# Optimization experiments

Measured on AMD Instinct MI355X. Metric: run time of the kernel, lower is better.

The kernel has to match this reference:

```python
import jax, jax.numpy as jnp
import numpy as np

B, T, D, H = 4, 2048, 512, 8
DH = D // H  # 64
EPS = 1e-5


def setup_inputs() -> dict:
    key = jax.random.key(0)
    ks = jax.random.split(key, 12)
    s = lambda k, shp, fan: jax.random.normal(k, shp, jnp.float32) * (fan ** -0.5)
    return {
        "x": jax.random.normal(ks[0], (B, T, D), jnp.float32),
        "ln1_g": jnp.ones((D,), jnp.float32),
        "ln1_b": jnp.zeros((D,), jnp.float32),
        "Wq": s(ks[1], (H, D, DH), D),  # per-head bias-free projections
        "Wk": s(ks[2], (H, D, DH), D),
        "Wv": s(ks[3], (H, D, DH), D),
        "Wproj": s(ks[4], (D, D), D),
        "bproj": jnp.zeros((D,), jnp.float32),
        "W1": s(ks[5], (D, 4 * D), D),
        "b1": jnp.zeros((4 * D,), jnp.float32),
        "W2": s(ks[6], (4 * D, D), 4 * D),
        "b2": jnp.zeros((D,), jnp.float32),
    }


def _layernorm(x, g, b):
    m = jnp.mean(x, axis=-1, keepdims=True)
    v = jnp.var(x, axis=-1, keepdims=True)
    return (x - m) * jax.lax.rsqrt(v + EPS) * g + b


def reference(x, ln1_g, ln1_b, Wq, Wk, Wv, Wproj, bproj, W1, b1, W2, b2):
    b, t, c = x.shape
    scale = c ** -0.5  # source scales by input channel dim, not head_size
    causal = jnp.tril(jnp.ones((t, t), bool))  # [T,T]

    # --- attention sublayer (pre-norm with ln1) ---
    h = _layernorm(x, ln1_g, ln1_b)
    q = jnp.einsum('btd,hde->bhte', h, Wq)
    k = jnp.einsum('btd,hde->bhte', h, Wk)
    v = jnp.einsum('btd,hde->bhte', h, Wv)
    scores = jnp.einsum('bhte,bhse->bhts', q, k) * scale  # [B,H,T,T]
    scores = jnp.where(causal, scores, -jnp.inf)
    att = jax.nn.softmax(scores, axis=-1)  # dropout = identity at inference
    o = jnp.einsum('bhts,bhse->bthe', att, v).reshape(b, t, c)  # concat heads
    sa = o @ Wproj + bproj
    x = x + sa

    # --- FFN sublayer (source reuses ln1, faithful) ---
    h2 = _layernorm(x, ln1_g, ln1_b)
    ff = jax.nn.relu(h2 @ W1 + b1) @ W2 + b2
    return x + ff
```

## Files before the change

### kernel.cpp

```cpp
#include <hip/hip_runtime.h>
#include <math.h>

#define B_ 4
#define T_ 2048
#define D_ 512
#define H_ 8
#define DH_ 64
#define BT_ 8192
#define FF_ 2048
#define EPS_ 1e-5f
#define SCALE_ 0.04419417382415922f
#define SC2_ 0.06375861151f
#define NEGINF_ -1e30f

typedef short b16x8 __attribute__((ext_vector_type(8)));
typedef short b16x4 __attribute__((ext_vector_type(4)));
typedef float f32x4 __attribute__((ext_vector_type(4)));

#define MFMA16(a, b, c) __builtin_amdgcn_mfma_f32_16x16x32_bf16(a, b, c, 0, 0, 0)
#define MFMA16K16(a, b, c) __builtin_amdgcn_mfma_f32_16x16x16bf16_1k(a, b, c, 0, 0, 0)

#define GLL16(gp, lp) \
    __builtin_amdgcn_global_load_lds((const __attribute__((address_space(1))) void*)(gp), \
                                     (__attribute__((address_space(3))) void*)(lp), 16, 0, 0)

#if __has_builtin(__builtin_amdgcn_exp2f)
#define EXP2F(x) __builtin_amdgcn_exp2f(x)
#else
#define EXP2F(x) exp2f(x)
#endif

static __device__ inline short f2bf(float f) {
    unsigned int u = __builtin_bit_cast(unsigned int, f);
    unsigned int r = (u + 0x7fffu + ((u >> 16) & 1u)) >> 16;
    return (short)r;
}
static __device__ inline short f2bf_trunc(float f) {
    return (short)(__builtin_bit_cast(unsigned int, f) >> 16);
}
static __device__ inline float bf2f(short s) {
    return __builtin_bit_cast(float, ((unsigned int)(unsigned short)s) << 16);
}

__global__ __launch_bounds__(256) void prologue_kernel(
        const float* __restrict__ Wq, const float* __restrict__ Wk,
        const float* __restrict__ Wv, const float* __restrict__ Wp,
        const float* __restrict__ W1, const float* __restrict__ W2,
        short* __restrict__ wqkv, short* __restrict__ wpt,
        short* __restrict__ w1t, short* __restrict__ w2t,
        const float* __restrict__ X, const float* __restrict__ G,
        const float* __restrict__ Bb, short* __restrict__ Y)
{
    __shared__ float tile[32][33];
    int idx = blockIdx.x;
    if (idx >= 3072) {
        int tid = threadIdx.y * 32 + threadIdx.x;
        int wave = tid >> 6, t = tid & 63;
        int row = (idx - 3072) * 4 + wave;
        const float* xr = X + (size_t)row * D_;
        float4 v0 = *(const float4*)(xr + t * 4);
        float4 v1 = *(const float4*)(xr + 256 + t * 4);
        float sum = v0.x + v0.y + v0.z + v0.w + v1.x + v1.y + v1.z + v1.w;
        float ssq = v0.x*v0.x + v0.y*v0.y + v0.z*v0.z + v0.w*v0.w
                  + v1.x*v1.x + v1.y*v1.y + v1.z*v1.z + v1.w*v1.w;
        #pragma unroll
        for (int off = 32; off > 0; off >>= 1) {
            sum += __shfl_down(sum, off);
            ssq += __shfl_down(ssq, off);
        }
        sum = __shfl(sum, 0);
        ssq = __shfl(ssq, 0);
        float mean = sum * (1.0f / D_);
        float var  = ssq * (1.0f / D_) - mean * mean;
        float rstd = rsqrtf(var + EPS_);
        float4 g0 = *(const float4*)(G + t * 4);
        float4 g1 = *(const float4*)(G + 256 + t * 4);
        float4 b0 = *(const float4*)(Bb + t * 4);
        float4 b1 = *(const float4*)(Bb + 256 + t * 4);
        short4 o0, o1;
        o0.x = f2bf((v0.x - mean) * rstd * g0.x + b0.x);
        o0.y = f2bf((v0.y - mean) * rstd * g0.y + b0.y);
        o0.z = f2bf((v0.z - mean) * rstd * g0.z + b0.z);
        o0.w = f2bf((v0.w - mean) * rstd * g0.w + b0.w);
        o1.x = f2bf((v1.x - mean) * rstd * g1.x + b1.x);
        o1.y = f2bf((v1.y - mean) * rstd * g1.y + b1.y);
        o1.z = f2bf((v1.z - mean) * rstd * g1.z + b1.z);
        o1.w = f2bf((v1.w - mean) * rstd * g1.w + b1.w);
        short* yr = Y + (size_t)row * D_;
        *(short4*)(yr + t * 4)       = o0;
        *(short4*)(yr + 256 + t * 4) = o1;
        return;
    }
    const float* src; short* dst; int R, C, tx0, ty0;
    if (idx < 768) {
        int w = idx >> 8, rem = idx & 255;
        int hh = rem >> 5, t = rem & 31;
        const float* base = (w == 0) ? Wq : ((w == 1) ? Wk : Wv);
        src = base + hh * (D_ * DH_);
        dst = wqkv + w * (512 * 512) + hh * (DH_ * D_);
        R = 512; C = 64; tx0 = (t & 1) * 32; ty0 = (t >> 1) * 32;
    } else if (idx < 1024) {
        int t = idx - 768;
        src = Wp; dst = wpt; R = 512; C = 512;
        tx0 = (t & 15) * 32; ty0 = (t >> 4) * 32;
    } else if (idx < 2048) {
        int t = idx - 1024;
        src = W1; dst = w1t; R = 512; C = 2048;
        tx0 = (t & 63) * 32; ty0 = (t >> 6) * 32;
    } else {
        int t = idx - 2048;
        src = W2; dst = w2t; R = 2048; C = 512;
        tx0 = (t & 15) * 32; ty0 = (t >> 4) * 32;
    }
    int tx = threadIdx.x, ty = threadIdx.y;
    #pragma unroll
    for (int i = 0; i < 32; i += 8)
        tile[ty + i][tx] = src[(size_t)(ty0 + ty + i) * C + tx0 + tx];
    __syncthreads();
    #pragma unroll
    for (int i = 0; i < 32; i += 8)
        dst[(size_t)(tx0 + ty + i) * R + ty0 + tx] = f2bf(tile[tx][ty + i]);
}

__global__ __launch_bounds__(256) void ln_bf16_kernel(const short* __restrict__ X,
        const float* __restrict__ G, const float* __restrict__ Bb,
        short* __restrict__ Y)
{
    int wave = threadIdx.x >> 6, t = threadIdx.x & 63;
    int row = blockIdx.x * 4 + wave;
    const short* xr = X + (size_t)row * D_ + t * 8;
    b16x8 xv = *(const b16x8*)xr;
    float v[8];
    float sum = 0.0f, ssq = 0.0f;
    #pragma unroll
    for (int e = 0; e < 8; ++e) {
        v[e] = bf2f(xv[e]);
        sum += v[e];
        ssq += v[e] * v[e];
    }
    #pragma unroll
    for (int off = 32; off > 0; off >>= 1) {
        sum += __shfl_down(sum, off);
        ssq += __shfl_down(ssq, off);
    }
    sum = __shfl(sum, 0);
    ssq = __shfl(ssq, 0);
    float mean = sum * (1.0f / D_);
    float var  = ssq * (1.0f / D_) - mean * mean;
    float rstd = rsqrtf(var + EPS_);

    float4 g0 = *(const float4*)(G + t * 8);
    float4 g1 = *(const float4*)(G + t * 8 + 4);
    float4 b0 = *(const float4*)(Bb + t * 8);
    float4 b1 = *(const float4*)(Bb + t * 8 + 4);
    float gg[8] = {g0.x, g0.y, g0.z, g0.w, g1.x, g1.y, g1.z, g1.w};
    float bb[8] = {b0.x, b0.y, b0.z, b0.w, b1.x, b1.y, b1.z, b1.w};
    b16x8 o;
    #pragma unroll
    for (int e = 0; e < 8; ++e)
        o[e] = f2bf((v[e] - mean) * rstd * gg[e] + bb[e]);
    *(b16x8*)(Y + (size_t)row * D_ + t * 8) = o;
}

__global__ __launch_bounds__(256) void mm64_kernel(const short* __restrict__ A,
        const short* __restrict__ Bt, void* __restrict__ C,
        const float* __restrict__ bias, const float* __restrict__ resid,
        int M, int N, int K, int relu, int out_bf16)
{
    __shared__ short As[2][128 * 32];
    __shared__ short Bs[2][64 * 32];
    const int tid = threadIdx.x;
    const int wave = tid >> 6, lane = tid & 63;
    const int quad = lane >> 4, l15 = lane & 15;
    const int m0 = blockIdx.x * 128, n0 = blockIdx.y * 64;
    const int mw = (wave & 1) * 64, nw = (wave >> 1) * 32;

#define STAGE_M64(bufi, kk) \
    { \
        for (int r = 0; r < 2; ++r) { \
            int c = r * 256 + tid; \
            int row = c >> 2, seg = (c & 3) ^ ((row >> 1) & 3); \
            GLL16(A + (size_t)(m0 + row) * K + (kk) + seg * 8, \
                  As[bufi] + (size_t)(r * 256 + wave * 64) * 8); \
        } \
        { \
            int row = tid >> 2, seg = (tid & 3) ^ ((row >> 1) & 3); \
            GLL16(Bt + (size_t)(n0 + row) * K + (kk) + seg * 8, \
                  Bs[bufi] + (size_t)(wave * 64) * 8); \
        } \
    }

    f32x4 acc[4][2];
    #pragma unroll
    for (int i = 0; i < 4; ++i)
        #pragma unroll
        for (int j = 0; j < 2; ++j)
            acc[i][j] = (f32x4){0.f, 0.f, 0.f, 0.f};

    STAGE_M64(0, 0);
    int buf = 0;
    for (int k0 = 0; k0 < K; k0 += 32) {
        __syncthreads();
        if (k0 + 32 < K) STAGE_M64(buf ^ 1, k0 + 32);
        b16x8 af[4], bf[2];
        #pragma unroll
        for (int i = 0; i < 4; ++i) {
            int row = mw + i * 16 + l15;
            af[i] = *(const b16x8*)(As[buf] + row * 32 + ((quad ^ ((row >> 1) & 3)) * 8));
        }
        #pragma unroll
        for (int j = 0; j < 2; ++j) {
            int row = nw + j * 16 + l15;
            bf[j] = *(const b16x8*)(Bs[buf] + row * 32 + ((quad ^ ((row >> 1) & 3)) * 8));
        }
        #pragma unroll
        for (int i = 0; i < 4; ++i)
            #pragma unroll
            for (int j = 0; j < 2; ++j)
                acc[i][j] = MFMA16(af[i], bf[j], acc[i][j]);
        buf ^= 1;
    }
#undef STAGE_M64

    #pragma unroll
    for (int i = 0; i < 4; ++i) {
        #pragma unroll
        for (int r = 0; r < 4; ++r) {
            size_t row = (size_t)(m0 + mw + i * 16 + quad * 4 + r);
            #pragma unroll
            for (int j = 0; j < 2; ++j) {
                int col = n0 + nw + j * 16 + l15;
                float v = acc[i][j][r];
                if (bias)  v += bias[col];
                if (resid) v += resid[row * N + col];
                if (relu)  v = fmaxf(v, 0.0f);
                if (out_bf16) ((short*)C)[row * N + col] = f2bf(v);
                else          ((float*)C)[row * N + col] = v;
            }
        }
    }
}

__global__ __launch_bounds__(256) void mm6464_kernel(const short* __restrict__ A,
        const short* __restrict__ Bt, void* __restrict__ C,
        const float* __restrict__ bias, const void* __restrict__ resid,
        int M, int N, int K, int relu, int out_bf16, int resid_bf16)
{
    __shared__ short As[2][64 * 64];
    __shared__ short Bs[2][64 * 64];
    const int tid = threadIdx.x;
    const int wave = tid >> 6, lane = tid & 63;
    const int quad = lane >> 4, l15 = lane & 15;
    const int m0 = blockIdx.x * 64, n0 = blockIdx.y * 64;
    const int nw = wave * 16;

#define STAGE_M66(bufi, kk) \
    { \
        for (int r = 0; r < 2; ++r) { \
            int c = r * 256 + tid; \
            int row = c >> 3, seg = (c & 7) ^ (row & 7); \
            GLL16(A + (size_t)(m0 + row) * K + (kk) + seg * 8, \
                  As[bufi] + (size_t)(r * 256 + wave * 64) * 8); \
            GLL16(Bt + (size_t)(n0 + row) * K + (kk) + seg * 8, \
                  Bs[bufi] + (size_t)(r * 256 + wave * 64) * 8); \
        } \
    }

    f32x4 acc[4];
    #pragma unroll
    for (int i = 0; i < 4; ++i) acc[i] = (f32x4){0.f, 0.f, 0.f, 0.f};

    STAGE_M66(0, 0);
    int buf = 0;
    for (int k0 = 0; k0 < K; k0 += 64) {
        __syncthreads();
        if (k0 + 64 < K) STAGE_M66(buf ^ 1, k0 + 64);
        b16x8 af[4][2], bf[2];
        #pragma unroll
        for (int i = 0; i < 4; ++i)
            #pragma unroll
            for (int kb = 0; kb < 2; ++kb) {
                int row = i * 16 + l15;
                af[i][kb] = *(const b16x8*)(As[buf] + row * 64 + (((kb * 4 + quad) ^ (row & 7)) * 8));
            }
        #pragma unroll
        for (int kb = 0; kb < 2; ++kb) {
            int row = nw + l15;
            bf[kb] = *(const b16x8*)(Bs[buf] + row * 64 + (((kb * 4 + quad) ^ (row & 7)) * 8));
        }
        #pragma unroll
        for (int kb = 0; kb < 2; ++kb)
            #pragma unroll
            for (int i = 0; i < 4; ++i)
                acc[i] = MFMA16(af[i][kb], bf[kb], acc[i]);
        buf ^= 1;
    }
#undef STAGE_M66

    #pragma unroll
    for (int i = 0; i < 4; ++i) {
        #pragma unroll
        for (int r = 0; r < 4; ++r) {
            size_t row = (size_t)(m0 + i * 16 + quad * 4 + r);
            int col = n0 + nw + l15;
            float v = acc[i][r];
            if (bias)  v += bias[col];
            if (resid) {
                if (resid_bf16) v += bf2f(((const short*)resid)[row * N + col]);
                else            v += ((const float*)resid)[row * N + col];
            }
            if (relu)  v = fmaxf(v, 0.0f);
            if (out_bf16) ((short*)C)[row * N + col] = f2bf(v);
            else          ((float*)C)[row * N + col] = v;
        }
    }
}

__global__ __launch_bounds__(256) void attn_kernel(const short* __restrict__ qkv,
        short* __restrict__ Opart, float* __restrict__ Ml)
{
    __shared__ short Qs[64 * 72];
    __shared__ short Ks[64 * 64];
    __shared__ short Vt[64 * 64];

    const int tid = threadIdx.x;
    const int wave = tid >> 6, lane = tid & 63;
    const int quad = lane >> 4, l15 = lane & 15;
    const int bh = blockIdx.x;
    const int qi = 31 - (int)blockIdx.y;
    const int split = blockIdx.z;
    const int b = bh >> 3, h = bh & 7;
    const size_t tok0 = (size_t)b * T_;
    const int qrow_rel = wave * 16 + l15;
    const int half = (qi + 1) >> 1;
    const int klo = split ? half : 0;
    const int khi = split ? qi + 1 : half;
    const int pidx = split * 1024 + bh * 32 + qi;
    short* Op = Opart + (size_t)pidx * 4096;
    float* mlp = Ml + (size_t)pidx * 64;

    if (klo >= khi) {
        for (int i = tid; i < 2048; i += 256) ((int*)Op)[i] = 0;
        if (tid < 64) mlp[tid] = 0.0f;
        return;
    }

    #pragma unroll
    for (int r = 0; r < 2; ++r) {
        int c = r * 256 + tid;
        int tk = c >> 3;
        int seg = (c & 7) ^ (tk & 7);
        GLL16(qkv + (tok0 + qi * 64 + tk) * 1536 + h * 64 + seg * 8,
              Qs + (size_t)(r * 256 + wave * 64) * 8);
    }

    float lrow = 0.0f;
    f32x4 ot[4];
    #pragma unroll
    for (int dt = 0; dt < 4; ++dt) ot[dt] = (f32x4){0.f, 0.f, 0.f, 0.f};

    b16x8 qf[2];

    for (int kj = klo; kj < khi; ++kj) {
        __syncthreads();
        #pragma unroll
        for (int r = 0; r < 2; ++r) {
            int c = r * 256 + tid;
            int tk = c >> 3;
            int seg = (c & 7) ^ (tk & 7);
            GLL16(qkv + (tok0 + kj * 64 + tk) * 1536 + 512 + h * 64 + seg * 8,
                  Ks + (size_t)(r * 256 + wave * 64) * 8);
        }
        {
            int s = tid >> 5, tp = tid & 31;
            const short* g0 = qkv + (tok0 + kj * 64 + tp * 2) * 1536 + 1024 + h * 64 + s * 8;
            b16x8 v0 = *(const b16x8*)g0;
            b16x8 v1 = *(const b16x8*)(g0 + 1536);
            int* vo = (int*)Vt;
            int gg = tp >> 1, hlf = tp & 1;
            #pragma unroll
            for (int e = 0; e < 8; ++e) {
                int row = s * 8 + e;
                unsigned int pk = (unsigned int)(unsigned short)v0[e]
                                | ((unsigned int)(unsigned short)v1[e] << 16);
                vo[row * 32 + ((gg ^ (row & 15)) << 1) + hlf] = pk;
            }
        }
        __syncthreads();

        if (kj == klo) {
            #pragma unroll
            for (int kb = 0; kb < 2; ++kb) {
                int row = wave * 16 + l15;
                qf[kb] = *(const b16x8*)(Qs + row * 64 + (((kb * 4 + quad) ^ (row & 7)) * 8));
            }
        }

        f32x4 st[4];
        #pragma unroll
        for (int mt = 0; mt < 4; ++mt) st[mt] = (f32x4){0.f, 0.f, 0.f, 0.f};
        #pragma unroll
        for (int mt = 0; mt < 4; ++mt) {
            int trow = mt * 16 + l15;
            #pragma unroll
            for (int kb = 0; kb < 2; ++kb) {
                b16x8 kf = *(const b16x8*)(Ks + trow * 64 + (((kb * 4 + quad) ^ (trow & 7)) * 8));
                st[mt] = MFMA16(kf, qf[kb], st[mt]);
            }
        }

        const bool diag = (kj == qi);
        float rs = 0.0f;
        b16x4 pf[4];
        #pragma unroll
        for (int mt = 0; mt < 4; ++mt)
            #pragma unroll
            for (int r = 0; r < 4; ++r) {
                float s = st[mt][r];
                if (diag && (mt * 16 + quad * 4 + r) > qrow_rel) s = NEGINF_;
                float e = EXP2F(s * SC2_);
                rs += e;
                pf[mt][r] = f2bf_trunc(e);
            }
        rs += __shfl_xor(rs, 16);
        rs += __shfl_xor(rs, 32);
        lrow += rs;
        #pragma unroll
        for (int dt = 0; dt < 4; ++dt) {
            const short* vrow = Vt + (dt * 16 + l15) * 64;
            #pragma unroll
            for (int kt = 0; kt < 4; ++kt) {
                b16x4 vf = *(const b16x4*)(vrow + (((kt * 4 + quad) ^ l15) << 2));
                ot[dt] = MFMA16K16(vf, pf[kt], ot[dt]);
            }
        }
    }

    __syncthreads();
    float inv = 1.0f / lrow;
    #pragma unroll
    for (int dt = 0; dt < 4; ++dt) {
        b16x4 o4;
        o4[0] = f2bf(ot[dt][0] * inv);
        o4[1] = f2bf(ot[dt][1] * inv);
        o4[2] = f2bf(ot[dt][2] * inv);
        o4[3] = f2bf(ot[dt][3] * inv);
        *(b16x4*)(Qs + (size_t)qrow_rel * 72 + dt * 16 + quad * 4) = o4;
    }
    {
        int row = tid >> 2, ch = tid & 3;
        b16x8 lo = *(const b16x8*)(Qs + (size_t)row * 72 + ch * 16);
        b16x8 hi = *(const b16x8*)(Qs + (size_t)row * 72 + ch * 16 + 8);
        short* dst = Op + row * 64 + ch * 16;
        *(b16x8*)dst = lo;
        *(b16x8*)(dst + 8) = hi;
    }
    if (quad == 0) mlp[qrow_rel] = lrow;
}

__global__ __launch_bounds__(256) void attn_combine_kernel(
        const short* __restrict__ Opart, const float* __restrict__ Ml,
        short* __restrict__ Ob)
{
    int pair = blockIdx.x;
    int bh = pair >> 5, qi = pair & 31;
    int b = bh >> 3, h = bh & 7;
    int tid = threadIdx.x;
    const short* O1 = Opart + (size_t)pair * 4096;
    const short* O2 = Opart + (size_t)(1024 + pair) * 4096;
    const float* ml1 = Ml + (size_t)pair * 64;
    const float* ml2 = Ml + (size_t)(1024 + pair) * 64;
    int ch = tid & 7;
    #pragma unroll
    for (int it = 0; it < 2; ++it) {
        int row = it * 32 + (tid >> 3);
        float l1 = ml1[row], l2 = ml2[row];
        float inv = 1.0f / (l1 + l2);
        float w1 = l1 * inv, w2 = l2 * inv;
        b16x8 a = *(const b16x8*)(O1 + row * 64 + ch * 8);
        b16x8 c = *(const b16x8*)(O2 + row * 64 + ch * 8);
        b16x8 o;
        #pragma unroll
        for (int e = 0; e < 8; ++e)
            o[e] = f2bf(w1 * bf2f(a[e]) + w2 * bf2f(c[e]));
        short* dst = Ob + ((size_t)(b * T_ + qi * 64 + row)) * 512 + h * 64 + ch * 8;
        *(b16x8*)dst = o;
    }
}

extern "C" void kernel_launch(void* const* d_in, const int* in_sizes, int n_in,
                              void* d_out, int out_size, void* d_ws, size_t ws_size,
                              hipStream_t stream) {
    (void)in_sizes; (void)n_in; (void)out_size; (void)ws_size;
    const float* x     = (const float*)d_in[0];
    const float* ln_g  = (const float*)d_in[1];
    const float* ln_b  = (const float*)d_in[2];
    const float* Wq    = (const float*)d_in[3];
    const float* Wk    = (const float*)d_in[4];
    const float* Wv    = (const float*)d_in[5];
    const float* Wproj = (const float*)d_in[6];
    const float* bproj = (const float*)d_in[7];
    const float* W1    = (const float*)d_in[8];
    const float* b1    = (const float*)d_in[9];
    const float* W2    = (const float*)d_in[10];
    const float* b2    = (const float*)d_in[11];
    float* out = (float*)d_out;

    char* W = (char*)d_ws;
    short* hbuf  = (short*)(W + 0);
    short* qkvb  = (short*)(W + ((size_t)8  << 20));
    short* attno = (short*)(W + ((size_t)32 << 20));
    short* x1b   = (short*)(W + ((size_t)40 << 20));
    short* ff1   = (short*)(W + ((size_t)56 << 20));
    short* wqkv  = (short*)(W + ((size_t)88 << 20));
    short* wpt   = (short*)(W + ((size_t)90 << 20));
    short* w1t   = (short*)(W + ((size_t)91 << 20));
    short* w2t   = (short*)(W + ((size_t)93 << 20));
    short* Opart = (short*)(W + ((size_t)96 << 20));
    float* Ml    = (float*)(W + ((size_t)112 << 20));

    prologue_kernel<<<dim3(3072 + BT_ / 4), dim3(32, 8), 0, stream>>>(
        Wq, Wk, Wv, Wproj, W1, W2, wqkv, wpt, w1t, w2t,
        x, ln_g, ln_b, hbuf);
    mm64_kernel<<<dim3(64, 24), dim3(256), 0, stream>>>(hbuf, wqkv, qkvb,
        nullptr, nullptr, BT_, 1536, D_, 0, 1);
    attn_kernel<<<dim3(32, 32, 2), dim3(256), 0, stream>>>(qkvb, Opart, Ml);
    attn_combine_kernel<<<dim3(1024), dim3(256), 0, stream>>>(Opart, Ml, attno);
    mm6464_kernel<<<dim3(128, 8), dim3(256), 0, stream>>>(attno, wpt, x1b,
        bproj, x, BT_, D_, D_, 0, 1, 0);
    ln_bf16_kernel<<<dim3(BT_ / 4), dim3(256), 0, stream>>>(x1b, ln_g, ln_b, hbuf);
    mm64_kernel<<<dim3(64, 32), dim3(256), 0, stream>>>(hbuf, w1t, ff1,
        b1, nullptr, BT_, FF_, D_, 1, 1);
    mm6464_kernel<<<dim3(128, 8), dim3(256), 0, stream>>>(ff1, w2t, out,
        b2, x1b, BT_, D_, FF_, 0, 0, 1);
}
```

Baseline: 257.2 us.

## Double-buffer K/V tiles in attention kernel to overlap loads with compute

```diff
diff --git a/kernel.cpp b/kernel.cpp
--- a/kernel.cpp
+++ b/kernel.cpp
@@ -319,9 +319,9 @@
 __global__ __launch_bounds__(256) void attn_kernel(const short* __restrict__ qkv,
         short* __restrict__ Opart, float* __restrict__ Ml)
 {
-    __shared__ short Qs[64 * 72];
-    __shared__ short Ks[64 * 64];
-    __shared__ short Vt[64 * 64];
+    __shared__ short Qs[64 * 64];
+    __shared__ short Ks[2][64 * 64];
+    __shared__ short Vt[2][64 * 64];
 
     const int tid = threadIdx.x;
     const int wave = tid >> 6, lane = tid & 63;
@@ -345,6 +345,12 @@
         return;
     }
 
+    const int s_ = tid >> 5, tp = tid & 31;
+    const int gg = tp >> 1, hlf = tp & 1;
+    const short* vbase = qkv + (tok0 + tp * 2) * 1536 + 1024 + h * 64 + s_ * 8;
+
+    b16x8 v0 = *(const b16x8*)(vbase + (size_t)klo * 64 * 1536);
+    b16x8 v1 = *(const b16x8*)(vbase + (size_t)klo * 64 * 1536 + 1536);
     #pragma unroll
     for (int r = 0; r < 2; ++r) {
         int c = r * 256 + tid;
@@ -352,6 +358,23 @@
         int seg = (c & 7) ^ (tk & 7);
         GLL16(qkv + (tok0 + qi * 64 + tk) * 1536 + h * 64 + seg * 8,
               Qs + (size_t)(r * 256 + wave * 64) * 8);
+        GLL16(qkv + (tok0 + klo * 64 + tk) * 1536 + 512 + h * 64 + seg * 8,
+              Ks[0] + (size_t)(r * 256 + wave * 64) * 8);
+    }
+    {
+        int* vo = (int*)Vt[0];
+        #pragma unroll
+        for (int e = 0; e < 8; ++e) {
+            int row = s_ * 8 + e;
+            unsigned int pk = (unsigned int)(unsigned short)v0[e]
+                            | ((unsigned int)(unsigned short)v1[e] << 16);
+            vo[row * 32 + ((gg ^ (row & 15)) << 1) + hlf] = pk;
+        }
+    }
+    {
+        int kv1 = (klo + 1 < khi) ? klo + 1 : klo;
+        v0 = *(const b16x8*)(vbase + (size_t)kv1 * 64 * 1536);
+        v1 = *(const b16x8*)(vbase + (size_t)kv1 * 64 * 1536 + 1536);
     }
 
     float lrow = 0.0f;
@@ -359,53 +382,50 @@
     #pragma unroll
     for (int dt = 0; dt < 4; ++dt) ot[dt] = (f32x4){0.f, 0.f, 0.f, 0.f};
 
+    __syncthreads();
+
     b16x8 qf[2];
-
-    for (int kj = klo; kj < khi; ++kj) {
-        __syncthreads();
-        #pragma unroll
-        for (int r = 0; r < 2; ++r) {
-            int c = r * 256 + tid;
-            int tk = c >> 3;
-            int seg = (c & 7) ^ (tk & 7);
-            GLL16(qkv + (tok0 + kj * 64 + tk) * 1536 + 512 + h * 64 + seg * 8,
-                  Ks + (size_t)(r * 256 + wave * 64) * 8);
-        }
-        {
-            int s = tid >> 5, tp = tid & 31;
-            const short* g0 = qkv + (tok0 + kj * 64 + tp * 2) * 1536 + 1024 + h * 64 + s * 8;
-            b16x8 v0 = *(const b16x8*)g0;
-            b16x8 v1 = *(const b16x8*)(g0 + 1536);
-            int* vo = (int*)Vt;
-            int gg = tp >> 1, hlf = tp & 1;
+    #pragma unroll
+    for (int kb = 0; kb < 2; ++kb) {
+        int row = wave * 16 + l15;
+        qf[kb] = *(const b16x8*)(Qs + row * 64 + (((kb * 4 + quad) ^ (row & 7)) * 8));
+    }
+
+    int cur = 0;
+    for (int kj = klo; kj < khi; ++kj, cur ^= 1) {
+        f32x4 st[4];
+        #pragma unroll
+        for (int mt = 0; mt < 4; ++mt) st[mt] = (f32x4){0.f, 0.f, 0.f, 0.f};
+        #pragma unroll
+        for (int mt = 0; mt < 4; ++mt) {
+            int trow = mt * 16 + l15;
+            #pragma unroll
+            for (int kb = 0; kb < 2; ++kb) {
+                b16x8 kf = *(const b16x8*)(Ks[cur] + trow * 64 + (((kb * 4 + quad) ^ (trow & 7)) * 8));
+                st[mt] = MFMA16(kf, qf[kb], st[mt]);
+            }
+        }
+
+        if (kj + 1 < khi) {
+            #pragma unroll
+            for (int r = 0; r < 2; ++r) {
+                int c = r * 256 + tid;
+                int tk = c >> 3;
+                int seg = (c & 7) ^ (tk & 7);
+                GLL16(qkv + (tok0 + (kj + 1) * 64 + tk) * 1536 + 512 + h * 64 + seg * 8,
+                      Ks[cur ^ 1] + (size_t)(r * 256 + wave * 64) * 8);
+            }
+            int* vo = (int*)Vt[cur ^ 1];
             #pragma unroll
             for (int e = 0; e < 8; ++e) {
-                int row = s * 8 + e;
+                int row = s_ * 8 + e;
                 unsigned int pk = (unsigned int)(unsigned short)v0[e]
                                 | ((unsigned int)(unsigned short)v1[e] << 16);
                 vo[row * 32 + ((gg ^ (row & 15)) << 1) + hlf] = pk;
             }
-        }
-        __syncthreads();
-
-        if (kj == klo) {
-            #pragma unroll
-            for (int kb = 0; kb < 2; ++kb) {
-                int row = wave * 16 + l15;
-                qf[kb] = *(const b16x8*)(Qs + row * 64 + (((kb * 4 + quad) ^ (row & 7)) * 8));
-            }
-        }
-
-        f32x4 st[4];
-        #pragma unroll
-        for (int mt = 0; mt < 4; ++mt) st[mt] = (f32x4){0.f, 0.f, 0.f, 0.f};
-        #pragma unroll
-        for (int mt = 0; mt < 4; ++mt) {
-            int trow = mt * 16 + l15;
-            #pragma unroll
-            for (int kb = 0; kb < 2; ++kb) {
-                b16x8 kf = *(const b16x8*)(Ks + trow * 64 + (((kb * 4 + quad) ^ (trow & 7)) * 8));
-                st[mt] = MFMA16(kf, qf[kb], st[mt]);
+            if (kj + 2 < khi) {
+                v0 = *(const b16x8*)(vbase + (size_t)(kj + 2) * 64 * 1536);
+                v1 = *(const b16x8*)(vbase + (size_t)(kj + 2) * 64 * 1536 + 1536);
             }
         }
 
@@ -416,28 +436,31 @@
         for (int mt = 0; mt < 4; ++mt)
             #pragma unroll
             for (int r = 0; r < 4; ++r) {
-                float s = st[mt][r];
-                if (diag && (mt * 16 + quad * 4 + r) > qrow_rel) s = NEGINF_;
-                float e = EXP2F(s * SC2_);
+                float sv = st[mt][r];
+                if (diag && (mt * 16 + quad * 4 + r) > qrow_rel) sv = NEGINF_;
+                float e = EXP2F(sv * SC2_);
                 rs += e;
                 pf[mt][r] = f2bf_trunc(e);
             }
         rs += __shfl_xor(rs, 16);
         rs += __shfl_xor(rs, 32);
         lrow += rs;
+
         #pragma unroll
         for (int dt = 0; dt < 4; ++dt) {
-            const short* vrow = Vt + (dt * 16 + l15) * 64;
+            const short* vrow = Vt[cur] + (dt * 16 + l15) * 64;
             #pragma unroll
             for (int kt = 0; kt < 4; ++kt) {
                 b16x4 vf = *(const b16x4*)(vrow + (((kt * 4 + quad) ^ l15) << 2));
                 ot[dt] = MFMA16K16(vf, pf[kt], ot[dt]);
             }
         }
-    }
-
-    __syncthreads();
+
+        __syncthreads();
+    }
+
     float inv = 1.0f / lrow;
+    short* strip = (short*)Ks;
     #pragma unroll
     for (int dt = 0; dt < 4; ++dt) {
         b16x4 o4;
@@ -445,12 +468,12 @@
         o4[1] = f2bf(ot[dt][1] * inv);
         o4[2] = f2bf(ot[dt][2] * inv);
         o4[3] = f2bf(ot[dt][3] * inv);
-        *(b16x4*)(Qs + (size_t)qrow_rel * 72 + dt * 16 + quad * 4) = o4;
+        *(b16x4*)(strip + (size_t)qrow_rel * 72 + dt * 16 + quad * 4) = o4;
     }
     {
         int row = tid >> 2, ch = tid & 3;
-        b16x8 lo = *(const b16x8*)(Qs + (size_t)row * 72 + ch * 16);
-        b16x8 hi = *(const b16x8*)(Qs + (size_t)row * 72 + ch * 16 + 8);
+        b16x8 lo = *(const b16x8*)(strip + (size_t)row * 72 + ch * 16);
+        b16x8 hi = *(const b16x8*)(strip + (size_t)row * 72 + ch * 16 + 8);
         short* dst = Op + row * 64 + ch * 16;
         *(b16x8*)dst = lo;
         *(b16x8*)(dst + 8) = hi;
```

Result: no change. 260.5 us (+1.3%).
